# Optimization experiments

Hardware: AMD Instinct MI355X
Metric: run time of the kernel (lower is better)

Reference implementation:

```python
import jax, jax.numpy as jnp
import numpy as np

T, NI, NK, F, H, O, E = 8, 20000, 50000, 128, 256, 128, 500000


def setup_inputs() -> dict:
    key = jax.random.key(0)
    ks = jax.random.split(key, 32)
    s = 0.05
    inp = {
        "x_inf": jax.random.normal(ks[0], (T, NI, F), jnp.float32),
        "x_item": jax.random.normal(ks[1], (T, NK, F), jnp.float32),
        "e1_src": jax.random.randint(ks[2], (T, E), 0, NI, jnp.int32),
        "e1_dst": jax.random.randint(ks[3], (T, E), 0, NK, jnp.int32),
        "e2_src": jax.random.randint(ks[4], (T, E), 0, NK, jnp.int32),
        "e2_dst": jax.random.randint(ks[5], (T, E), 0, NI, jnp.int32),
        "target_idx": 1234,
        # layer 1, edge type a: influencer -> item (dst = item)
        "W1a_l": s * jax.random.normal(ks[6], (H, F), jnp.float32),
        "b1a_l": jnp.zeros((H,), jnp.float32),
        "W1a_r": s * jax.random.normal(ks[7], (H, F), jnp.float32),
        # layer 1, edge type b: item -> influencer (dst = influencer)
        "W1b_l": s * jax.random.normal(ks[8], (H, F), jnp.float32),
        "b1b_l": jnp.zeros((H,), jnp.float32),
        "W1b_r": s * jax.random.normal(ks[9], (H, F), jnp.float32),
        # layer 2, edge type a (dst = item; output unused by the model head, grads are zero)
        "W2a_l": s * jax.random.normal(ks[10], (O, H), jnp.float32),
        "b2a_l": jnp.zeros((O,), jnp.float32),
        "W2a_r": s * jax.random.normal(ks[11], (O, H), jnp.float32),
        # layer 2, edge type b (dst = influencer)
        "W2b_l": s * jax.random.normal(ks[12], (O, H), jnp.float32),
        "b2b_l": jnp.zeros((O,), jnp.float32),
        "W2b_r": s * jax.random.normal(ks[13], (O, H), jnp.float32),
        # GRU (PyTorch gate order: r, z, n)
        "W_ih": s * jax.random.normal(ks[14], (3 * H, O), jnp.float32),
        "W_hh": s * jax.random.normal(ks[15], (3 * H, H), jnp.float32),
        "b_ih": jnp.zeros((3 * H,), jnp.float32),
        "b_hh": jnp.zeros((3 * H,), jnp.float32),
        # attention + prediction head
        "W_att": s * jax.random.normal(ks[16], (1, H), jnp.float32),
        "b_att": jnp.zeros((1,), jnp.float32),
        "W_p1": s * jax.random.normal(ks[17], (H // 2, H), jnp.float32),
        "b_p1": jnp.zeros((H // 2,), jnp.float32),
        "W_p2": s * jax.random.normal(ks[18], (1, H // 2), jnp.float32),
        "b_p2": jnp.zeros((1,), jnp.float32),
    }
    return inp


def _sage(x_src, x_dst, src, dst, Wl, bl, Wr, n_dst):
    # PyG SAGEConv: lin_l(mean_j x_j) + lin_r(x_i); lin_l has bias, lin_r does not
    msg = x_src[src]                                            # [E, F]
    agg = jax.ops.segment_sum(msg, dst, num_segments=n_dst)     # [n_dst, F]
    cnt = jax.ops.segment_sum(jnp.ones_like(dst, dtype=x_src.dtype), dst, num_segments=n_dst)
    mean = agg / jnp.maximum(cnt, 1.0)[:, None]
    return mean @ Wl.T + bl + x_dst @ Wr.T


def reference(x_inf, x_item, e1_src, e1_dst, e2_src, e2_dst, target_idx,
              W1a_l, b1a_l, W1a_r, W1b_l, b1b_l, W1b_r,
              W2a_l, b2a_l, W2a_r, W2b_l, b2b_l, W2b_r,
              W_ih, W_hh, b_ih, b_hh, W_att, b_att, W_p1, b_p1, W_p2, b_p2):
    def step(carry, xs):
        xi, xk, s1, d1, s2, d2 = xs
        # hetero conv1 (aggr='sum' over edge types; each dst type has one incoming edge type)
        h_item = jax.nn.relu(_sage(xi, xk, s1, d1, W1a_l, b1a_l, W1a_r, NK))
        h_inf = jax.nn.relu(_sage(xk, xi, s2, d2, W1b_l, b1b_l, W1b_r, NI))
        # conv2: only the influencer output feeds the head (item output is dead code)
        o_inf = _sage(h_item, h_inf, s2, d2, W2b_l, b2b_l, W2b_r, NI)
        return carry, o_inf[target_idx]

    _, seq = jax.lax.scan(step, None, (x_inf, x_item, e1_src, e1_dst, e2_src, e2_dst))  # [T, O]

    def gru_step(h, x):
        gi = x @ W_ih.T + b_ih
        gh = h @ W_hh.T + b_hh
        i_r, i_z, i_n = jnp.split(gi, 3)
        h_r, h_z, h_n = jnp.split(gh, 3)
        r = jax.nn.sigmoid(i_r + h_r)
        z = jax.nn.sigmoid(i_z + h_z)
        n = jnp.tanh(i_n + r * h_n)
        h_new = (1.0 - z) * n + z * h
        return h_new, h_new

    h0 = jnp.zeros((H,), seq.dtype)
    _, rnn = jax.lax.scan(gru_step, h0, seq)                    # [T, H]

    att = jax.nn.softmax(rnn @ W_att.T + b_att, axis=0)         # [T, 1]
    ctx = jnp.sum(att * rnn, axis=0)                            # [H]
    hid = jax.nn.relu(ctx @ W_p1.T + b_p1)
    score = (hid @ W_p2.T + b_p2)[0]
    return score
```

## Files before the change

kernel.cpp:

```cpp
#include <hip/hip_runtime.h>
#include <math.h>

#define T 8
#define NI 20000
#define NK 50000
#define F 128
#define H 256
#define O 128
#define E 500000
#define G3 (3*H)
#define MAXS 256
#define CAP1 256
#define BMW 1568
#define NB 8
#define RPB 32
#define EQ (E/4)
#define SENT 0xFFFFFFFFu

#define OFF_CNT2   0
#define OFF_ITEMS  32
#define OFF_CNT1   (32 + T*MAXS*4)
#define OFF_HSUM   (OFF_CNT1 + T*MAXS*4)
#define OFF_Z2SUM  (OFF_HSUM + T*H*4)
#define OFF_GBM    (OFF_Z2SUM + T*F*4)
#define WS_ZERO    (OFF_GBM + T*BMW*4)
#define OFF_LIST1  WS_ZERO
#define OFF_RNN    (OFF_LIST1 + (size_t)T*MAXS*CAP1*4)
#define OFF_OWS    (OFF_RNN + T*H*4)
#define WS_USED    (OFF_OWS + T*O*4)

__global__ void k_find_e2(const int* __restrict__ e2_src, const int* __restrict__ e2_dst,
                          const int* __restrict__ target_p,
                          int* __restrict__ cnt2, int* __restrict__ items,
                          unsigned* __restrict__ gbm) {
    int t = blockIdx.y;
    long q = (long)blockIdx.x * 256 + threadIdx.x;
    if (q >= EQ) return;
    int target = *target_p;
    const int4 d4 = ((const int4*)(e2_dst + (long)t * E))[q];
    int dd[4] = {d4.x, d4.y, d4.z, d4.w};
#pragma unroll
    for (int c = 0; c < 4; ++c) {
        if (dd[c] == target) {
            long j = q * 4 + c;
            int src = e2_src[(long)t * E + j];
            int pos = atomicAdd(&cnt2[t], 1);
            if (pos < MAXS) {
                items[t * MAXS + pos] = src;
                atomicOr(&gbm[t * BMW + (src >> 5)], 1u << (src & 31));
            }
        }
    }
}

__global__ void k_scan_e1(const int* __restrict__ e1_src, const int* __restrict__ e1_dst,
                          const int* __restrict__ cnt2, const int* __restrict__ items,
                          const unsigned* __restrict__ gbm,
                          int* __restrict__ cnt1, int* __restrict__ list1) {
    int t = blockIdx.y;
    long q = (long)blockIdx.x * 256 + threadIdx.x;
    if (q >= EQ) return;
    const unsigned* bm = gbm + t * BMW;
    const int4 d4 = ((const int4*)(e1_dst + (long)t * E))[q];
    int dd[4] = {d4.x, d4.y, d4.z, d4.w};
#pragma unroll
    for (int c = 0; c < 4; ++c) {
        int d = dd[c];
        if (!((bm[d >> 5] >> (d & 31)) & 1u)) continue;
        long j = q * 4 + c;
        int src = e1_src[(long)t * E + j];
        int ns = min(cnt2[t], MAXS);
        for (int i = 0; i < ns; ++i) {
            if (items[t * MAXS + i] == d) {
                int pos = atomicAdd(&cnt1[t * MAXS + i], 1);
                if (pos < CAP1) list1[((long)t * MAXS + i) * CAP1 + pos] = src;
            }
        }
    }
}

__global__ void k_hitem(const float* __restrict__ x_item, const float* __restrict__ x_inf,
                        const float* __restrict__ W1a_l, const float* __restrict__ b1a_l,
                        const float* __restrict__ W1a_r,
                        const int* __restrict__ cnt2, const int* __restrict__ items,
                        const int* __restrict__ cnt1, const int* __restrict__ list1,
                        float* __restrict__ hsum, float* __restrict__ z2sum) {
    int t = blockIdx.y, slot = blockIdx.x;
    int ns = min(cnt2[t], MAXS);
    if (slot >= ns) return;
    __shared__ float z1[F], xk[F];
    int item = items[t * MAXS + slot];
    int ne = cnt1[t * MAXS + slot];
    float inv = 1.0f / fmaxf((float)ne, 1.0f);
    int nr = min(ne, CAP1);
    if (threadIdx.x < F) {
        int f = threadIdx.x;
        const int* lst = list1 + ((long)t * MAXS + slot) * CAP1;
        float s = 0.0f;
        for (int e = 0; e < nr; ++e)
            s += x_inf[((long)t * NI + lst[e]) * F + f];
        z1[f] = s * inv;
        float xv = x_item[((long)t * NK + item) * F + f];
        xk[f] = xv;
        atomicAdd(&z2sum[t * F + f], xv);
    }
    __syncthreads();
    int h = threadIdx.x;
    float acc = b1a_l[h];
    const float* wl = W1a_l + h * F;
    const float* wr = W1a_r + h * F;
    for (int f = 0; f < F; ++f) acc += z1[f] * wl[f] + xk[f] * wr[f];
    acc = fmaxf(acc, 0.0f);
    atomicAdd(&hsum[t * H + h], acc);
}

__global__ void __launch_bounds__(256, 1)
k_gru(const float* __restrict__ x_inf, const int* __restrict__ target_p,
      const float* __restrict__ W1b_l, const float* __restrict__ b1b_l,
      const float* __restrict__ W1b_r,
      const float* __restrict__ W2b_l, const float* __restrict__ b2b_l,
      const float* __restrict__ W2b_r,
      const int* __restrict__ cnt2,
      const float* __restrict__ hsum, const float* __restrict__ z2sum,
      const float* __restrict__ W_ih, const float* __restrict__ b_ih,
      const float* __restrict__ W_hh, const float* __restrict__ b_hh,
      const float* __restrict__ W_att, const float* __restrict__ b_att,
      const float* __restrict__ W_p1, const float* __restrict__ b_p1,
      const float* __restrict__ W_p2, const float* __restrict__ b_p2,
      float* __restrict__ rnn, float* __restrict__ o_ws, float* __restrict__ out) {
    __shared__ float w[3 * RPB][H];
    __shared__ float h[H];
    __shared__ float srnn[T][H];
    __shared__ float satt[T], tmp[H], hid[128];
    __shared__ float z2[F], xt[F], hinf[H], mh[H];
    __shared__ float so_all[T][O];
    __shared__ float sgi[T][3][RPB];
    int b = blockIdx.x, tid = threadIdx.x;
    int wv = tid >> 6, lane = tid & 63;
    unsigned* rnn_u = (unsigned*)rnn;
    unsigned* o_u = (unsigned*)o_ws;

    {
        int t = b;
        int target = *target_p;
        float c2 = fmaxf((float)cnt2[t], 1.0f);
        if (tid < F) {
            z2[tid] = z2sum[t * F + tid] / c2;
            xt[tid] = x_inf[((long)t * NI + target) * F + tid];
        }
        mh[tid] = hsum[t * H + tid] / c2;
        __syncthreads();
        for (int r = wv; r < H; r += 4) {
            float wl0 = W1b_l[r * F + lane], wl1 = W1b_l[r * F + 64 + lane];
            float wr0 = W1b_r[r * F + lane], wr1 = W1b_r[r * F + 64 + lane];
            float s = wl0 * z2[lane] + wl1 * z2[lane + 64]
                    + wr0 * xt[lane] + wr1 * xt[lane + 64];
            for (int off = 32; off; off >>= 1) s += __shfl_down(s, off);
            if (lane == 0) hinf[r] = fmaxf(s + b1b_l[r], 0.0f);
        }
        __syncthreads();
        for (int r = wv; r < O; r += 4) {
            float s = 0.0f;
            for (int c = 0; c < 4; ++c) {
                int k = lane + 64 * c;
                s += W2b_l[r * H + k] * mh[k] + W2b_r[r * H + k] * hinf[k];
            }
            for (int off = 32; off; off >>= 1) s += __shfl_down(s, off);
            if (lane == 0)
                __hip_atomic_store(&o_u[t * O + r], __float_as_uint(s + b2b_l[r]),
                                   __ATOMIC_RELAXED, __HIP_MEMORY_SCOPE_AGENT);
        }
    }

    for (int idx = tid; idx < 3 * RPB * H; idx += 256) {
        int r = idx >> 8, k = idx & 255;
        int g = r / RPB, j = r - g * RPB;
        w[r][k] = W_hh[((long)(g * H + b * RPB + j)) * H + k];
    }

    for (int idx = tid; idx < T * O; idx += 256) {
        unsigned v;
        do {
            v = __hip_atomic_load(&o_u[idx], __ATOMIC_RELAXED,
                                  __HIP_MEMORY_SCOPE_AGENT);
            if (v != SENT) break;
            __builtin_amdgcn_s_sleep(1);
        } while (true);
        so_all[idx >> 7][idx & 127] = __uint_as_float(v);
    }
    h[tid] = 0.0f;
    __syncthreads();

    for (int lr = wv; lr < 3 * RPB; lr += 4) {
        int g = lr >> 5, j = lr & 31;
        int r = g * H + b * RPB + j;
        float w0 = W_ih[(long)r * O + lane];
        float w1 = W_ih[(long)r * O + 64 + lane];
        float bi = b_ih[r];
        for (int t = 0; t < T; ++t) {
            float s = w0 * so_all[t][lane] + w1 * so_all[t][lane + 64];
            for (int off = 32; off; off >>= 1) s += __shfl_down(s, off);
            if (lane == 0) sgi[t][g][j] = s + bi;
        }
    }
    __syncthreads();

    for (int t = 0; t < T; ++t) {
        for (int j = wv; j < RPB; j += 4) {
            float sr = 0.f, sz = 0.f, sn = 0.f;
            for (int c = 0; c < 4; ++c) {
                int k = lane + 64 * c;
                float hk = h[k];
                sr += w[j][k] * hk;
                sz += w[RPB + j][k] * hk;
                sn += w[2 * RPB + j][k] * hk;
            }
            for (int off = 32; off; off >>= 1) {
                sr += __shfl_down(sr, off);
                sz += __shfl_down(sz, off);
                sn += __shfl_down(sn, off);
            }
            if (lane == 0) {
                int i = b * RPB + j;
                float r = 1.0f / (1.0f + expf(-(sgi[t][0][j] + sr + b_hh[i])));
                float z = 1.0f / (1.0f + expf(-(sgi[t][1][j] + sz + b_hh[H + i])));
                float n = tanhf(sgi[t][2][j] + r * (sn + b_hh[2 * H + i]));
                float hn = (1.0f - z) * n + z * h[i];
                __hip_atomic_store(&rnn_u[t * H + i], __float_as_uint(hn),
                                   __ATOMIC_RELAXED, __HIP_MEMORY_SCOPE_AGENT);
            }
        }
        __syncthreads();
        unsigned v;
        do {
            v = __hip_atomic_load(&rnn_u[t * H + tid], __ATOMIC_RELAXED,
                                  __HIP_MEMORY_SCOPE_AGENT);
            if (v != SENT) break;
            __builtin_amdgcn_s_sleep(1);
        } while (true);
        float hv = __uint_as_float(v);
        h[tid] = hv;
        srnn[t][tid] = hv;
        __syncthreads();
    }
    if (b != 0) return;
    {
        int tt = tid >> 5, l32 = tid & 31;
        float a = 0.f;
        for (int c = 0; c < 8; ++c) {
            int k = l32 + 32 * c;
            a += W_att[k] * srnn[tt][k];
        }
        for (int off = 16; off; off >>= 1) a += __shfl_down(a, off, 32);
        if (l32 == 0) satt[tt] = a + b_att[0];
    }
    __syncthreads();
    if (tid == 0) {
        float m = satt[0];
        for (int t = 1; t < T; ++t) m = fmaxf(m, satt[t]);
        float s = 0.f;
        for (int t = 0; t < T; ++t) { satt[t] = expf(satt[t] - m); s += satt[t]; }
        for (int t = 0; t < T; ++t) satt[t] /= s;
    }
    __syncthreads();
    {
        float ctx = 0.f;
        for (int t = 0; t < T; ++t) ctx += satt[t] * srnn[t][tid];
        tmp[tid] = ctx;
    }
    __syncthreads();
    for (int r = wv; r < 128; r += 4) {
        float s = 0.0f;
        for (int c = 0; c < 4; ++c) {
            int k = lane + 64 * c;
            s += W_p1[r * H + k] * tmp[k];
        }
        for (int off = 32; off; off >>= 1) s += __shfl_down(s, off);
        if (lane == 0) hid[r] = fmaxf(s + b_p1[r], 0.0f);
    }
    __syncthreads();
    if (tid < 64) {
        float s = W_p2[lane] * hid[lane] + W_p2[lane + 64] * hid[lane + 64];
        for (int off = 32; off; off >>= 1) s += __shfl_down(s, off);
        if (lane == 0) out[0] = s + b_p2[0];
    }
}

extern "C" void kernel_launch(void* const* d_in, const int* in_sizes, int n_in,
                              void* d_out, int out_size, void* d_ws, size_t ws_size,
                              hipStream_t stream) {
    const float* x_inf  = (const float*)d_in[0];
    const float* x_item = (const float*)d_in[1];
    const int* e1_src = (const int*)d_in[2];
    const int* e1_dst = (const int*)d_in[3];
    const int* e2_src = (const int*)d_in[4];
    const int* e2_dst = (const int*)d_in[5];
    const int* target_p = (const int*)d_in[6];
    const float* W1a_l = (const float*)d_in[7];
    const float* b1a_l = (const float*)d_in[8];
    const float* W1a_r = (const float*)d_in[9];
    const float* W1b_l = (const float*)d_in[10];
    const float* b1b_l = (const float*)d_in[11];
    const float* W1b_r = (const float*)d_in[12];
    const float* W2b_l = (const float*)d_in[16];
    const float* b2b_l = (const float*)d_in[17];
    const float* W2b_r = (const float*)d_in[18];
    const float* W_ih = (const float*)d_in[19];
    const float* W_hh = (const float*)d_in[20];
    const float* b_ih = (const float*)d_in[21];
    const float* b_hh = (const float*)d_in[22];
    const float* W_att = (const float*)d_in[23];
    const float* b_att = (const float*)d_in[24];
    const float* W_p1 = (const float*)d_in[25];
    const float* b_p1 = (const float*)d_in[26];
    const float* W_p2 = (const float*)d_in[27];
    const float* b_p2 = (const float*)d_in[28];
    float* out = (float*)d_out;

    char* ws = (char*)d_ws;
    int*      cnt2  = (int*)(ws + OFF_CNT2);
    int*      items = (int*)(ws + OFF_ITEMS);
    int*      cnt1  = (int*)(ws + OFF_CNT1);
    float*    hsum  = (float*)(ws + OFF_HSUM);
    float*    z2sum = (float*)(ws + OFF_Z2SUM);
    unsigned* gbm   = (unsigned*)(ws + OFF_GBM);
    int*      list1 = (int*)(ws + OFF_LIST1);
    float*    rnn   = (float*)(ws + OFF_RNN);
    float*    o_ws  = (float*)(ws + OFF_OWS);

    hipMemsetAsync(d_ws, 0, WS_ZERO, stream);
    hipMemsetAsync(ws + OFF_RNN, 0xFF, (T * H + T * O) * 4, stream);

    dim3 g1((EQ + 255) / 256, T);
    k_find_e2<<<g1, 256, 0, stream>>>(e2_src, e2_dst, target_p, cnt2, items, gbm);

    k_scan_e1<<<g1, 256, 0, stream>>>(e1_src, e1_dst, cnt2, items, gbm, cnt1, list1);

    dim3 g3(MAXS, T);
    k_hitem<<<g3, 256, 0, stream>>>(x_item, x_inf, W1a_l, b1a_l, W1a_r,
                                    cnt2, items, cnt1, list1, hsum, z2sum);

    k_gru<<<NB, 256, 0, stream>>>(x_inf, target_p,
                                  W1b_l, b1b_l, W1b_r, W2b_l, b2b_l, W2b_r,
                                  cnt2, hsum, z2sum, W_ih, b_ih, W_hh, b_hh,
                                  W_att, b_att, W_p1, b_p1, W_p2, b_p2,
                                  rnn, o_ws, out);
}
```

Baseline: 663.7 us.

## Replace cross-block spin-sync GRU with single-block GRU and split layer2/gi kernels

The 8-block GRU kernel that synchronised through global-memory sentinel spin-waits is replaced by separate kernels: a per-timestep layer-2 kernel, a parallel input-gate kernel, and a single 1024-thread GRU block. That block reads a transposed W_hh, prepared by a new transpose kernel, with coalesced per-thread column dot products. This removes the inter-block polling and the sentinel memset. In exchange it adds kernel launches, and the recurrence now runs on one CU that streams W_hh from global/L2 on every step.

```diff
diff --git a/kernel.cpp b/kernel.cpp
--- a/kernel.cpp
+++ b/kernel.cpp
@@ -12,10 +12,7 @@
 #define MAXS 256
 #define CAP1 256
 #define BMW 1568
-#define NB 8
-#define RPB 32
 #define EQ (E/4)
-#define SENT 0xFFFFFFFFu
 
 #define OFF_CNT2   0
 #define OFF_ITEMS  32
@@ -25,9 +22,25 @@
 #define OFF_GBM    (OFF_Z2SUM + T*F*4)
 #define WS_ZERO    (OFF_GBM + T*BMW*4)
 #define OFF_LIST1  WS_ZERO
-#define OFF_RNN    (OFF_LIST1 + (size_t)T*MAXS*CAP1*4)
-#define OFF_OWS    (OFF_RNN + T*H*4)
-#define WS_USED    (OFF_OWS + T*O*4)
+#define OFF_O      (OFF_LIST1 + (size_t)T*MAXS*CAP1*4)
+#define OFF_GI     (OFF_O + T*O*4)
+#define OFF_WHHT   (OFF_GI + T*G3*4)
+#define WS_USED    (OFF_WHHT + (size_t)H*G3*4)
+
+__global__ void k_prep(const float* __restrict__ W_hh, float* __restrict__ W_hhT) {
+    __shared__ float tile[64][65];
+    int r0 = blockIdx.x * 64;
+    int k0 = blockIdx.y * 64;
+    for (int idx = threadIdx.x; idx < 64 * 64; idx += 256) {
+        int r = idx >> 6, k = idx & 63;
+        tile[r][k] = W_hh[(long)(r0 + r) * H + k0 + k];
+    }
+    __syncthreads();
+    for (int idx = threadIdx.x; idx < 64 * 64; idx += 256) {
+        int k = idx >> 6, r = idx & 63;
+        W_hhT[(long)(k0 + k) * G3 + r0 + r] = tile[r][k];
+    }
+}
 
 __global__ void k_find_e2(const int* __restrict__ e2_src, const int* __restrict__ e2_dst,
                           const int* __restrict__ target_p,
@@ -114,137 +127,107 @@
     atomicAdd(&hsum[t * H + h], acc);
 }
 
-__global__ void __launch_bounds__(256, 1)
-k_gru(const float* __restrict__ x_inf, const int* __restrict__ target_p,
-      const float* __restrict__ W1b_l, const float* __restrict__ b1b_l,
-      const float* __restrict__ W1b_r,
-      const float* __restrict__ W2b_l, const float* __restrict__ b2b_l,
-      const float* __restrict__ W2b_r,
-      const int* __restrict__ cnt2,
-      const float* __restrict__ hsum, const float* __restrict__ z2sum,
-      const float* __restrict__ W_ih, const float* __restrict__ b_ih,
-      const float* __restrict__ W_hh, const float* __restrict__ b_hh,
+__global__ void k_layer2(const float* __restrict__ x_inf, const int* __restrict__ target_p,
+                         const float* __restrict__ W1b_l, const float* __restrict__ b1b_l,
+                         const float* __restrict__ W1b_r,
+                         const float* __restrict__ W2b_l, const float* __restrict__ b2b_l,
+                         const float* __restrict__ W2b_r,
+                         const int* __restrict__ cnt2,
+                         const float* __restrict__ hsum, const float* __restrict__ z2sum,
+                         float* __restrict__ o_ws) {
+    int t = blockIdx.x, tid = threadIdx.x;
+    int wv = tid >> 6, lane = tid & 63;
+    __shared__ float z2[F], xt[F], hinf[H], mh[H];
+    int target = *target_p;
+    float c2 = fmaxf((float)cnt2[t], 1.0f);
+    if (tid < F) {
+        z2[tid] = z2sum[t * F + tid] / c2;
+        xt[tid] = x_inf[((long)t * NI + target) * F + tid];
+    }
+    mh[tid] = hsum[t * H + tid] / c2;
+    __syncthreads();
+    for (int r = wv; r < H; r += 4) {
+        float wl0 = W1b_l[r * F + lane], wl1 = W1b_l[r * F + 64 + lane];
+        float wr0 = W1b_r[r * F + lane], wr1 = W1b_r[r * F + 64 + lane];
+        float s = wl0 * z2[lane] + wl1 * z2[lane + 64]
+                + wr0 * xt[lane] + wr1 * xt[lane + 64];
+        for (int off = 32; off; off >>= 1) s += __shfl_down(s, off);
+        if (lane == 0) hinf[r] = fmaxf(s + b1b_l[r], 0.0f);
+    }
+    __syncthreads();
+    for (int r = wv; r < O; r += 4) {
+        float s = 0.0f;
+        for (int c = 0; c < 4; ++c) {
+            int k = lane + 64 * c;
+            s += W2b_l[r * H + k] * mh[k] + W2b_r[r * H + k] * hinf[k];
+        }
+        for (int off = 32; off; off >>= 1) s += __shfl_down(s, off);
+        if (lane == 0) o_ws[t * O + r] = s + b2b_l[r];
+    }
+}
+
+__global__ void k_gi(const float* __restrict__ o_ws, const float* __restrict__ W_ih,
+                     const float* __restrict__ b_ih, float* __restrict__ gi) {
+    int t = blockIdx.y;
+    int wv = threadIdx.x >> 6, lane = threadIdx.x & 63;
+    int row = blockIdx.x * 4 + wv;
+    const float* w = W_ih + (long)row * O;
+    const float* x = o_ws + t * O;
+    float s = w[lane] * x[lane] + w[lane + 64] * x[lane + 64];
+    for (int off = 32; off; off >>= 1) s += __shfl_down(s, off);
+    if (lane == 0) gi[t * G3 + row] = s + b_ih[row];
+}
+
+__global__ void __launch_bounds__(1024, 1)
+k_gru(const float* __restrict__ gi_g, const float* __restrict__ W_hhT,
+      const float* __restrict__ b_hh,
       const float* __restrict__ W_att, const float* __restrict__ b_att,
       const float* __restrict__ W_p1, const float* __restrict__ b_p1,
       const float* __restrict__ W_p2, const float* __restrict__ b_p2,
-      float* __restrict__ rnn, float* __restrict__ o_ws, float* __restrict__ out) {
-    __shared__ float w[3 * RPB][H];
-    __shared__ float h[H];
+      float* __restrict__ out) {
+    __shared__ float sgi[T][G3];
+    __shared__ float sbhh[G3];
+    __shared__ float gh[G3];
+    __shared__ float hs[H];
     __shared__ float srnn[T][H];
     __shared__ float satt[T], tmp[H], hid[128];
-    __shared__ float z2[F], xt[F], hinf[H], mh[H];
-    __shared__ float so_all[T][O];
-    __shared__ float sgi[T][3][RPB];
-    int b = blockIdx.x, tid = threadIdx.x;
-    int wv = tid >> 6, lane = tid & 63;
-    unsigned* rnn_u = (unsigned*)rnn;
-    unsigned* o_u = (unsigned*)o_ws;
-
-    {
-        int t = b;
-        int target = *target_p;
-        float c2 = fmaxf((float)cnt2[t], 1.0f);
-        if (tid < F) {
-            z2[tid] = z2sum[t * F + tid] / c2;
-            xt[tid] = x_inf[((long)t * NI + target) * F + tid];
-        }
-        mh[tid] = hsum[t * H + tid] / c2;
+    int tid = threadIdx.x;
+    for (int i = tid; i < T * G3; i += 1024) sgi[i / G3][i % G3] = gi_g[i];
+    for (int i = tid; i < G3; i += 1024) sbhh[i] = b_hh[i];
+    if (tid < H) hs[tid] = 0.0f;
+    __syncthreads();
+
+    for (int t = 0; t < T; ++t) {
+        if (tid < G3) {
+            float g = 0.0f;
+            if (t > 0) {
+                const float* wp = W_hhT + tid;
+                float a0 = 0.f, a1 = 0.f, a2 = 0.f, a3 = 0.f;
+#pragma unroll 8
+                for (int k = 0; k < H; k += 4) {
+                    a0 += wp[(k + 0) * G3] * hs[k + 0];
+                    a1 += wp[(k + 1) * G3] * hs[k + 1];
+                    a2 += wp[(k + 2) * G3] * hs[k + 2];
+                    a3 += wp[(k + 3) * G3] * hs[k + 3];
+                }
+                g = (a0 + a1) + (a2 + a3);
+            }
+            gh[tid] = g;
+        }
         __syncthreads();
-        for (int r = wv; r < H; r += 4) {
-            float wl0 = W1b_l[r * F + lane], wl1 = W1b_l[r * F + 64 + lane];
-            float wr0 = W1b_r[r * F + lane], wr1 = W1b_r[r * F + 64 + lane];
-            float s = wl0 * z2[lane] + wl1 * z2[lane + 64]
-                    + wr0 * xt[lane] + wr1 * xt[lane + 64];
-            for (int off = 32; off; off >>= 1) s += __shfl_down(s, off);
-            if (lane == 0) hinf[r] = fmaxf(s + b1b_l[r], 0.0f);
+        if (tid < H) {
+            int i = tid;
+            float r = 1.0f / (1.0f + expf(-(sgi[t][i] + gh[i] + sbhh[i])));
+            float z = 1.0f / (1.0f + expf(-(sgi[t][H + i] + gh[H + i] + sbhh[H + i])));
+            float n = tanhf(sgi[t][2 * H + i] + r * (gh[2 * H + i] + sbhh[2 * H + i]));
+            float hn = (1.0f - z) * n + z * hs[i];
+            hs[i] = hn;
+            srnn[t][i] = hn;
         }
         __syncthreads();
-        for (int r = wv; r < O; r += 4) {
-            float s = 0.0f;
-            for (int c = 0; c < 4; ++c) {
-                int k = lane + 64 * c;
-                s += W2b_l[r * H + k] * mh[k] + W2b_r[r * H + k] * hinf[k];
-            }
-            for (int off = 32; off; off >>= 1) s += __shfl_down(s, off);
-            if (lane == 0)
-                __hip_atomic_store(&o_u[t * O + r], __float_as_uint(s + b2b_l[r]),
-                                   __ATOMIC_RELAXED, __HIP_MEMORY_SCOPE_AGENT);
-        }
-    }
-
-    for (int idx = tid; idx < 3 * RPB * H; idx += 256) {
-        int r = idx >> 8, k = idx & 255;
-        int g = r / RPB, j = r - g * RPB;
-        w[r][k] = W_hh[((long)(g * H + b * RPB + j)) * H + k];
-    }
-
-    for (int idx = tid; idx < T * O; idx += 256) {
-        unsigned v;
-        do {
-            v = __hip_atomic_load(&o_u[idx], __ATOMIC_RELAXED,
-                                  __HIP_MEMORY_SCOPE_AGENT);
-            if (v != SENT) break;
-            __builtin_amdgcn_s_sleep(1);
-        } while (true);
-        so_all[idx >> 7][idx & 127] = __uint_as_float(v);
-    }
-    h[tid] = 0.0f;
-    __syncthreads();
-
-    for (int lr = wv; lr < 3 * RPB; lr += 4) {
-        int g = lr >> 5, j = lr & 31;
-        int r = g * H + b * RPB + j;
-        float w0 = W_ih[(long)r * O + lane];
-        float w1 = W_ih[(long)r * O + 64 + lane];
-        float bi = b_ih[r];
-        for (int t = 0; t < T; ++t) {
-            float s = w0 * so_all[t][lane] + w1 * so_all[t][lane + 64];
-            for (int off = 32; off; off >>= 1) s += __shfl_down(s, off);
-            if (lane == 0) sgi[t][g][j] = s + bi;
-        }
-    }
-    __syncthreads();
-
-    for (int t = 0; t < T; ++t) {
-        for (int j = wv; j < RPB; j += 4) {
-            float sr = 0.f, sz = 0.f, sn = 0.f;
-            for (int c = 0; c < 4; ++c) {
-                int k = lane + 64 * c;
-                float hk = h[k];
-                sr += w[j][k] * hk;
-                sz += w[RPB + j][k] * hk;
-                sn += w[2 * RPB + j][k] * hk;
-            }
-            for (int off = 32; off; off >>= 1) {
-                sr += __shfl_down(sr, off);
-                sz += __shfl_down(sz, off);
-                sn += __shfl_down(sn, off);
-            }
-            if (lane == 0) {
-                int i = b * RPB + j;
-                float r = 1.0f / (1.0f + expf(-(sgi[t][0][j] + sr + b_hh[i])));
-                float z = 1.0f / (1.0f + expf(-(sgi[t][1][j] + sz + b_hh[H + i])));
-                float n = tanhf(sgi[t][2][j] + r * (sn + b_hh[2 * H + i]));
-                float hn = (1.0f - z) * n + z * h[i];
-                __hip_atomic_store(&rnn_u[t * H + i], __float_as_uint(hn),
-                                   __ATOMIC_RELAXED, __HIP_MEMORY_SCOPE_AGENT);
-            }
-        }
-        __syncthreads();
-        unsigned v;
-        do {
-            v = __hip_atomic_load(&rnn_u[t * H + tid], __ATOMIC_RELAXED,
-                                  __HIP_MEMORY_SCOPE_AGENT);
-            if (v != SENT) break;
-            __builtin_amdgcn_s_sleep(1);
-        } while (true);
-        float hv = __uint_as_float(v);
-        h[tid] = hv;
-        srnn[t][tid] = hv;
-        __syncthreads();
-    }
-    if (b != 0) return;
-    {
+    }
+
+    if (tid < 256) {
         int tt = tid >> 5, l32 = tid & 31;
         float a = 0.f;
         for (int c = 0; c < 8; ++c) {
@@ -263,26 +246,29 @@
         for (int t = 0; t < T; ++t) satt[t] /= s;
     }
     __syncthreads();
-    {
+    if (tid < H) {
         float ctx = 0.f;
         for (int t = 0; t < T; ++t) ctx += satt[t] * srnn[t][tid];
         tmp[tid] = ctx;
     }
     __syncthreads();
-    for (int r = wv; r < 128; r += 4) {
-        float s = 0.0f;
-        for (int c = 0; c < 4; ++c) {
-            int k = lane + 64 * c;
-            s += W_p1[r * H + k] * tmp[k];
-        }
+    {
+        int wv = tid >> 6, lane = tid & 63;
+        for (int r = wv; r < 128; r += 16) {
+            float s = 0.0f;
+            for (int c = 0; c < 4; ++c) {
+                int k = lane + 64 * c;
+                s += W_p1[(long)r * H + k] * tmp[k];
+            }
+            for (int off = 32; off; off >>= 1) s += __shfl_down(s, off);
+            if (lane == 0) hid[r] = fmaxf(s + b_p1[r], 0.0f);
+        }
+    }
+    __syncthreads();
+    if (tid < 64) {
+        float s = W_p2[tid] * hid[tid] + W_p2[tid + 64] * hid[tid + 64];
         for (int off = 32; off; off >>= 1) s += __shfl_down(s, off);
-        if (lane == 0) hid[r] = fmaxf(s + b_p1[r], 0.0f);
-    }
-    __syncthreads();
-    if (tid < 64) {
-        float s = W_p2[lane] * hid[lane] + W_p2[lane + 64] * hid[lane + 64];
-        for (int off = 32; off; off >>= 1) s += __shfl_down(s, off);
-        if (lane == 0) out[0] = s + b_p2[0];
+        if (tid == 0) out[0] = s + b_p2[0];
     }
 }
 
@@ -325,11 +311,13 @@
     float*    z2sum = (float*)(ws + OFF_Z2SUM);
     unsigned* gbm   = (unsigned*)(ws + OFF_GBM);
     int*      list1 = (int*)(ws + OFF_LIST1);
-    float*    rnn   = (float*)(ws + OFF_RNN);
-    float*    o_ws  = (float*)(ws + OFF_OWS);
+    float*    o_ws  = (float*)(ws + OFF_O);
+    float*    gi    = (float*)(ws + OFF_GI);
+    float*    whhT  = (float*)(ws + OFF_WHHT);
 
     hipMemsetAsync(d_ws, 0, WS_ZERO, stream);
-    hipMemsetAsync(ws + OFF_RNN, 0xFF, (T * H + T * O) * 4, stream);
+
+    k_prep<<<dim3(12, 4), 256, 0, stream>>>(W_hh, whhT);
 
     dim3 g1((EQ + 255) / 256, T);
     k_find_e2<<<g1, 256, 0, stream>>>(e2_src, e2_dst, target_p, cnt2, items, gbm);
@@ -340,9 +328,12 @@
     k_hitem<<<g3, 256, 0, stream>>>(x_item, x_inf, W1a_l, b1a_l, W1a_r,
                                     cnt2, items, cnt1, list1, hsum, z2sum);
 
-    k_gru<<<NB, 256, 0, stream>>>(x_inf, target_p,
-                                  W1b_l, b1b_l, W1b_r, W2b_l, b2b_l, W2b_r,
-                                  cnt2, hsum, z2sum, W_ih, b_ih, W_hh, b_hh,
-                                  W_att, b_att, W_p1, b_p1, W_p2, b_p2,
-                                  rnn, o_ws, out);
-}
+    k_layer2<<<T, 256, 0, stream>>>(x_inf, target_p, W1b_l, b1b_l, W1b_r,
+                                    W2b_l, b2b_l, W2b_r, cnt2, hsum, z2sum, o_ws);
+
+    dim3 g5(G3 / 4, T);
+    k_gi<<<g5, 256, 0, stream>>>(o_ws, W_ih, b_ih, gi);
+
+    k_gru<<<1, 1024, 0, stream>>>(gi, whhT, b_hh, W_att, b_att,
+                                  W_p1, b_p1, W_p2, b_p2, out);
+}
```

After: 581.5 us. -12.4%, faster.
